# Performance work log

Measured on AMD Instinct MI355X. Metric: run time of the kernel, lower is better.

## Reference

```python
import jax, jax.numpy as jnp
import numpy as np
import math

B, S, E = 2, 4096, 2048
H, HKV, DK, DV = 16, 4, 128, 128
WIN = 512
EPS = 1e-5
NEG = -1e30


def setup_inputs() -> dict:
    key = jax.random.key(0)
    ks = jax.random.split(key, 8)
    scale = 1.0 / math.sqrt(E)
    return {
        "embeddings": jax.random.normal(ks[0], (B, S, E), dtype=jnp.float32),
        "cos_buffer": jax.random.uniform(ks[1], (2, 1, S, DK), dtype=jnp.float32),
        "sin_buffer": jax.random.uniform(ks[2], (2, 1, S, DK), dtype=jnp.float32),
        "wq": jax.random.normal(ks[3], (E, H * DK), dtype=jnp.float32) * scale,
        "wk": jax.random.normal(ks[4], (E, HKV * DK), dtype=jnp.float32) * scale,
        "wv": jax.random.normal(ks[5], (E, HKV * DV), dtype=jnp.float32) * scale,
        "wo": jax.random.normal(ks[6], (H * DV, E), dtype=jnp.float32) * (1.0 / math.sqrt(H * DV)),
        "window_size": WIN,
    }


def _rotate(f, cos, sin):
    half = f.shape[-1] // 2
    swapped = jnp.concatenate([f[..., half:], f[..., :half]], axis=-1)
    return cos * f + sin * swapped


def reference(embeddings, cos_buffer, sin_buffer, wq, wk, wv, wo, window_size):
    b, s, _ = embeddings.shape
    normed = embeddings * jax.lax.rsqrt(
        jnp.mean(jnp.square(embeddings), axis=-1, keepdims=True) + EPS)
    q = (normed @ wq).reshape(b, s, H, DK).transpose(0, 2, 1, 3)
    k = (normed @ wk).reshape(b, s, HKV, DK).transpose(0, 2, 1, 3)
    v = (normed @ wv).reshape(b, s, HKV, DV).transpose(0, 2, 1, 3)

    q = _rotate(q, cos_buffer[0], sin_buffer[0])
    k = _rotate(k, cos_buffer[1], sin_buffer[1])

    g = H // HKV
    k = jnp.repeat(k, g, axis=1)
    v = jnp.repeat(v, g, axis=1)

    W = window_size
    nb = s // W
    qb = q.reshape(b, H, nb, W, DK)
    kb = k.reshape(b, H, nb, W, DK)
    vb = v.reshape(b, H, nb, W, DV)
    k_prev = jnp.pad(kb, ((0, 0), (0, 0), (1, 0), (0, 0), (0, 0)))[:, :, :nb]
    v_prev = jnp.pad(vb, ((0, 0), (0, 0), (1, 0), (0, 0), (0, 0)))[:, :, :nb]
    kcat = jnp.concatenate([k_prev, kb], axis=3)
    vcat = jnp.concatenate([v_prev, vb], axis=3)

    scores = jnp.einsum('bhnqd,bhnkd->bhnqk', qb, kcat) / math.sqrt(DK)

    i = jnp.arange(W)[:, None]
    j = jnp.arange(2 * W)[None, :]
    base = (j > i) & (j <= i + W)
    blk = jnp.arange(nb)[:, None, None]
    mask = base[None] & ((blk > 0) | (j[None] >= W))
    scores = jnp.where(mask[None, None], scores, NEG)

    probs = jax.nn.softmax(scores, axis=-1)
    out = jnp.einsum('bhnqk,bhnkd->bhnqd', probs, vcat)
    out = out.reshape(b, H, s, DV).transpose(0, 2, 1, 3).reshape(b, s, H * DV)
    out = out @ wo
    return embeddings + out
```

## Files before the change

kernel.cpp:

```cpp
#include <hip/hip_runtime.h>

typedef unsigned short u16;
typedef __attribute__((ext_vector_type(8))) short s16x8;
typedef __attribute__((ext_vector_type(8))) unsigned short u16x8;
typedef __attribute__((ext_vector_type(4))) unsigned short u16x4;
typedef __attribute__((ext_vector_type(4))) float f32x4;

#define DEV __device__ __forceinline__

DEV u16 f2bf(float x) {
  union { float f; unsigned u; } c; c.f = x;
  unsigned r = c.u + 0x7FFFu + ((c.u >> 16) & 1u);
  return (u16)(r >> 16);
}
DEV float bf2f(u16 u) {
  union { unsigned u; float f; } c; c.u = ((unsigned)u) << 16;
  return c.f;
}
DEV void gload_lds16(const void* g, void* l) {
  __builtin_amdgcn_global_load_lds((const __attribute__((address_space(1))) void*)g,
                                   (__attribute__((address_space(3))) void*)l, 16, 0, 0);
}

__global__ __launch_bounds__(256) void k_rmsnorm(const float* __restrict__ emb, u16* __restrict__ X) {
  const int row = blockIdx.x;
  const int t = threadIdx.x;
  const float4* p4 = (const float4*)(emb + (size_t)row * 2048);
  float4 v0 = p4[t * 2], v1 = p4[t * 2 + 1];
  float ss = v0.x * v0.x + v0.y * v0.y + v0.z * v0.z + v0.w * v0.w
           + v1.x * v1.x + v1.y * v1.y + v1.z * v1.z + v1.w * v1.w;
  for (int off = 32; off; off >>= 1) ss += __shfl_xor(ss, off);
  __shared__ float red[4];
  if ((t & 63) == 0) red[t >> 6] = ss;
  __syncthreads();
  float tot = red[0] + red[1] + red[2] + red[3];
  float inv = rsqrtf(tot * (1.0f / 2048.0f) + 1e-5f);
  float v[8] = {v0.x, v0.y, v0.z, v0.w, v1.x, v1.y, v1.z, v1.w};
  u16x8 o;
  for (int j = 0; j < 8; ++j) o[j] = f2bf(v[j] * inv);
  *(u16x8*)(X + (size_t)row * 2048 + t * 8) = o;
}

__global__ __launch_bounds__(256) void k_transpose(const float* __restrict__ src, u16* __restrict__ dst,
                                                   int C, int dstStride) {
  __shared__ float tile[32][33];
  const int bc = blockIdx.x * 32, br = blockIdx.y * 32;
  const int tx = threadIdx.x & 31, ty = threadIdx.x >> 5;
  for (int i = 0; i < 32; i += 8)
    tile[ty + i][tx] = src[(size_t)(br + ty + i) * C + bc + tx];
  __syncthreads();
  for (int i = 0; i < 32; i += 8)
    dst[(size_t)(bc + ty + i) * dstStride + br + tx] = f2bf(tile[tx][ty + i]);
}

template <int EPI>
__global__ __launch_bounds__(512) void k_gemm256(const u16* __restrict__ A, const u16* __restrict__ Bt,
                                                 const int N, const int K, const int NBN,
                                                 const float* __restrict__ cosb, const float* __restrict__ sinb,
                                                 u16* __restrict__ Qb, u16* __restrict__ Kb,
                                                 u16* __restrict__ VtOut,
                                                 const float* __restrict__ Emb, float* __restrict__ Cf) {
  __shared__ u16 Asm[2][256 * 64];
  __shared__ u16 Bsm[2][256 * 64];
  const int t = threadIdx.x, w = t >> 6, l = t & 63, g = (l >> 4), cc = l & 15;
  const int wm = w >> 2, wn = w & 3;

  const int lin = blockIdx.x;
  const int bm = lin / NBN, bn = lin % NBN;
  const size_t m0 = (size_t)bm * 256, n0 = (size_t)bn * 256;

  const int srow = t >> 3, sch = t & 7;

  auto stA = [&](int kt, int p, int pass) {
    const int row = pass * 64 + srow;
    const int c2 = sch ^ (row & 7);
    gload_lds16(A + (m0 + row) * K + kt * 64 + c2 * 8, &Asm[p][row * 64 + sch * 8]);
  };
  auto stB = [&](int kt, int p, int pass) {
    const int row = pass * 64 + srow;
    const int c2 = sch ^ (row & 7);
    gload_lds16(Bt + (n0 + row) * K + kt * 64 + c2 * 8, &Bsm[p][row * 64 + sch * 8]);
  };

  f32x4 acc[8][4];
#pragma unroll
  for (int mi = 0; mi < 8; ++mi)
#pragma unroll
    for (int ni = 0; ni < 4; ++ni) acc[mi][ni] = (f32x4){0.f, 0.f, 0.f, 0.f};

  const int NT = K >> 6;
#pragma unroll
  for (int pass = 0; pass < 4; ++pass) { stA(0, 0, pass); stB(0, 0, pass); }
  __syncthreads();

  for (int kt = 0; kt < NT; ++kt) {
    const int p = kt & 1;
    const bool pf = (kt + 1 < NT);
    const u16* Ap = &Asm[p][0];
    const u16* Bp = &Bsm[p][0];

    s16x8 bf[2][4];
#pragma unroll
    for (int kk = 0; kk < 2; ++kk)
#pragma unroll
      for (int ni = 0; ni < 4; ++ni) {
        const int row = wn * 16 + ni * 64 + cc;
        bf[kk][ni] = *(const s16x8*)&Bp[row * 64 + (((kk * 4 + g) ^ (row & 7)) * 8)];
      }

#pragma unroll
    for (int q = 0; q < 4; ++q) {
      s16x8 af[2][2];
#pragma unroll
      for (int kk = 0; kk < 2; ++kk)
#pragma unroll
        for (int m2 = 0; m2 < 2; ++m2) {
          const int row = wm * 128 + (q * 2 + m2) * 16 + cc;
          af[kk][m2] = *(const s16x8*)&Ap[row * 64 + (((kk * 4 + g) ^ (row & 7)) * 8)];
        }
      if (pf) {
        if (q == 0) { stA(kt + 1, p ^ 1, 0); stA(kt + 1, p ^ 1, 1); stB(kt + 1, p ^ 1, 0); }
        else if (q == 1) { stA(kt + 1, p ^ 1, 2); stA(kt + 1, p ^ 1, 3); stB(kt + 1, p ^ 1, 1); }
        else if (q == 2) { stB(kt + 1, p ^ 1, 2); stB(kt + 1, p ^ 1, 3); }
      }
#pragma unroll
      for (int m2 = 0; m2 < 2; ++m2)
#pragma unroll
        for (int ni = 0; ni < 4; ++ni)
#pragma unroll
          for (int kk = 0; kk < 2; ++kk)
            acc[q * 2 + m2][ni] =
                __builtin_amdgcn_mfma_f32_16x16x32_bf16(af[kk][m2], bf[kk][ni], acc[q * 2 + m2][ni], 0, 0, 0);
    }
    __syncthreads();
  }

  if (EPI == 1) {
#pragma unroll
    for (int mi = 0; mi < 8; ++mi)
#pragma unroll
      for (int ni = 0; ni < 4; ++ni)
#pragma unroll
        for (int r = 0; r < 4; ++r) {
          const size_t row = m0 + wm * 128 + mi * 16 + g * 4 + r;
          const size_t col = n0 + wn * 16 + ni * 64 + cc;
          Cf[row * N + col] = acc[mi][ni][r] + Emb[row * N + col];
        }
  } else if ((int)n0 < 2560) {
    const bool isK = (int)n0 >= 2048;
    const float* cbase = cosb + (isK ? 524288 : 0);
    const float* sbase = sinb + (isK ? 524288 : 0);
    const int dlo = wn * 16 + cc;
#pragma unroll
    for (int mi = 0; mi < 8; ++mi)
#pragma unroll
      for (int p = 0; p < 2; ++p) {
        const int colbase = (int)n0 + p * 128;
#pragma unroll
        for (int r = 0; r < 4; ++r) {
          const int row = (int)m0 + wm * 128 + mi * 16 + g * 4 + r;
          const int bb = row >> 12, s = row & 4095;
          const float lo = acc[mi][2 * p + 0][r];
          const float hi = acc[mi][2 * p + 1][r];
          const float* cpr = cbase + (size_t)s * 128;
          const float* spr = sbase + (size_t)s * 128;
          const u16 olo = f2bf(cpr[dlo] * lo + spr[dlo] * hi);
          const u16 ohi = f2bf(cpr[dlo + 64] * hi + spr[dlo + 64] * lo);
          if (!isK) {
            const int h = colbase >> 7;
            u16* dq = Qb + ((size_t)(bb * 16 + h) * 4096 + s) * 128;
            dq[dlo] = olo;
            dq[dlo + 64] = ohi;
          } else {
            const int hkv = (colbase - 2048) >> 7;
            u16* dk = Kb + ((size_t)(bb * 4 + hkv) * 4096 + s) * 128;
            dk[dlo] = olo;
            dk[dlo + 64] = ohi;
          }
        }
      }
  } else {
    const int bb = (int)(m0 >> 12);
    const int s0base = (int)(m0 & 4095);
#pragma unroll
    for (int mi = 0; mi < 8; ++mi)
#pragma unroll
      for (int ni = 0; ni < 4; ++ni) {
        const int dcol = (int)(n0 - 2560) + wn * 16 + ni * 64 + cc;
        const int hkv = dcol >> 7, d = dcol & 127;
        const int s = s0base + wm * 128 + mi * 16 + g * 4;
        u16x4 o;
#pragma unroll
        for (int r = 0; r < 4; ++r) o[r] = f2bf(acc[mi][ni][r]);
        *(u16x4*)(VtOut + ((size_t)(bb * 4 + hkv) * 128 + d) * 4096 + s) = o;
      }
  }
}

__global__ __launch_bounds__(256) void k_attn(const u16* __restrict__ Q, const u16* __restrict__ K,
                                              const u16* __restrict__ Vt, u16* __restrict__ AO) {
  const int bid = blockIdx.x;
  const int lin = (bid & 7) * 128 + (bid >> 3);
  const int grp = lin >> 7;
  const int b = grp >> 2, hkv = grp & 3;
  const int rem = lin & 127;
  const int h = hkv * 4 + (rem >> 5);
  const int qt = rem & 31;

  const int t = threadIdx.x, w = t >> 6, l = t & 63, g = l >> 4, cc = l & 15;
  const int q0 = qt * 128;
  const int myq0 = q0 + w * 32;
  const u16* Qp = Q + (((size_t)b * 16 + h) * 4096 + q0) * 128;
  const u16* Kp = K + ((size_t)b * 4 + hkv) * 4096 * 128;
  const u16* Vp = Vt + ((size_t)b * 4 + hkv) * 128 * 4096;

  __shared__ u16 Kl[2][32 * 128];
  __shared__ u16 Vl[2][128 * 32];
  __shared__ u16 Ps[4][32 * 40];
  u16* myPs = &Ps[w][0];

  auto stage = [&](int kt, int bufi) {
    for (int pass = 0; pass < 2; ++pass) {
      const int m = pass * 256 + t;
      const int row = m >> 4, cst = m & 15;
      const int cor = cst ^ (row & 7);
      gload_lds16(Kp + (size_t)(kt * 32 + row) * 128 + cor * 8, &Kl[bufi][m * 8]);
    }
    for (int pass = 0; pass < 2; ++pass) {
      const int m = pass * 256 + t;
      const int d = m >> 2, cst = m & 3;
      const int cor = cst ^ (d & 3);
      gload_lds16(Vp + (size_t)d * 4096 + kt * 32 + cor * 8, &Vl[bufi][m * 8]);
    }
  };

  s16x8 qf[2][4];
  for (int mi = 0; mi < 2; ++mi)
    for (int kk = 0; kk < 4; ++kk)
      qf[mi][kk] = *(const s16x8*)(Qp + (size_t)(w * 32 + mi * 16 + cc) * 128 + kk * 32 + g * 8);

  f32x4 accO[2][8];
  for (int mi = 0; mi < 2; ++mi)
    for (int nd = 0; nd < 8; ++nd) accO[mi][nd] = (f32x4){0.f, 0.f, 0.f, 0.f};
  float mrun[2], lrun[2];
  for (int mi = 0; mi < 2; ++mi) { mrun[mi] = -1e30f; lrun[mi] = 0.f; }

  int lo = q0 - 511; if (lo < 0) lo = 0;
  const int kt_lo = lo >> 5, kt_hi = (q0 + 127) >> 5;
  const float scale = 0.08838834764831845f;

  int cur = 0;
  stage(kt_lo, 0);
  __syncthreads();

  for (int kt = kt_lo; kt <= kt_hi; ++kt) {
    if (kt < kt_hi) stage(kt + 1, cur ^ 1);

    const int k0 = kt * 32;
    const bool haswork = (k0 <= myq0 + 31) && (k0 + 31 >= myq0 - 511);
    const bool fullw   = (k0 + 31 <= myq0) && (k0 >= myq0 - 480);

    if (haswork) {
      f32x4 sc[2][2];
      for (int mi = 0; mi < 2; ++mi)
        for (int nk = 0; nk < 2; ++nk) sc[mi][nk] = (f32x4){0.f, 0.f, 0.f, 0.f};
      __builtin_amdgcn_s_setprio(1);
      for (int kk = 0; kk < 4; ++kk) {
        s16x8 kb[2];
        for (int nk = 0; nk < 2; ++nk) {
          const int row = nk * 16 + cc;
          kb[nk] = *(const s16x8*)&Kl[cur][row * 128 + (((kk * 4 + g) ^ (row & 7)) * 8)];
        }
        for (int mi = 0; mi < 2; ++mi)
          for (int nk = 0; nk < 2; ++nk)
            sc[mi][nk] = __builtin_amdgcn_mfma_f32_16x16x32_bf16(kb[nk], qf[mi][kk], sc[mi][nk], 0, 0, 0);
      }
      __builtin_amdgcn_s_setprio(0);

      for (int mi = 0; mi < 2; ++mi) {
        const int qpos = myq0 + mi * 16 + cc;
        if (fullw) {
          for (int nk = 0; nk < 2; ++nk)
            for (int r = 0; r < 4; ++r) sc[mi][nk][r] *= scale;
        } else {
          for (int nk = 0; nk < 2; ++nk)
            for (int r = 0; r < 4; ++r) {
              const int kpos = k0 + nk * 16 + g * 4 + r;
              const float v = sc[mi][nk][r] * scale;
              sc[mi][nk][r] = (kpos <= qpos && kpos + 512 > qpos) ? v : -1e30f;
            }
        }
        float rm = sc[mi][0][0];
        for (int nk = 0; nk < 2; ++nk)
          for (int r = 0; r < 4; ++r) rm = fmaxf(rm, sc[mi][nk][r]);
        rm = fmaxf(rm, __shfl_xor(rm, 16));
        rm = fmaxf(rm, __shfl_xor(rm, 32));
        const float mnew = fmaxf(mrun[mi], rm);
        float rs = 0.f;
        if (fullw) {
          for (int nk = 0; nk < 2; ++nk)
            for (int r = 0; r < 4; ++r) {
              float pv = __expf(sc[mi][nk][r] - mnew);
              sc[mi][nk][r] = pv;
              rs += pv;
            }
        } else {
          for (int nk = 0; nk < 2; ++nk)
            for (int r = 0; r < 4; ++r) {
              float pv = sc[mi][nk][r];
              pv = (pv <= -1e29f) ? 0.f : __expf(pv - mnew);
              sc[mi][nk][r] = pv;
              rs += pv;
            }
        }
        rs += __shfl_xor(rs, 16);
        rs += __shfl_xor(rs, 32);
        const float alpha = __expf(mrun[mi] - mnew);
        mrun[mi] = mnew;
        lrun[mi] = lrun[mi] * alpha + rs;
        for (int nd = 0; nd < 8; ++nd)
          for (int r = 0; r < 4; ++r) accO[mi][nd][r] *= alpha;
        for (int nk = 0; nk < 2; ++nk) {
          u16x4 o;
          for (int r = 0; r < 4; ++r) o[r] = f2bf(sc[mi][nk][r]);
          *(u16x4*)&myPs[(mi * 16 + cc) * 40 + nk * 16 + g * 4] = o;
        }
      }

      __builtin_amdgcn_s_setprio(1);
      {
        s16x8 pa[2];
        for (int mi = 0; mi < 2; ++mi)
          pa[mi] = *(const s16x8*)&myPs[(mi * 16 + cc) * 40 + g * 8];
        for (int nd = 0; nd < 8; ++nd) {
          const int d = nd * 16 + cc;
          s16x8 vb = *(const s16x8*)&Vl[cur][d * 32 + ((g ^ (d & 3)) * 8)];
          for (int mi = 0; mi < 2; ++mi)
            accO[mi][nd] = __builtin_amdgcn_mfma_f32_16x16x32_bf16(vb, pa[mi], accO[mi][nd], 0, 0, 0);
        }
      }
      __builtin_amdgcn_s_setprio(0);
    }

    __syncthreads();
    cur ^= 1;
  }

  u16* op = AO + ((size_t)b * 4096 + q0) * 2048 + (size_t)h * 128;
  for (int mi = 0; mi < 2; ++mi) {
    const float inv = 1.0f / lrun[mi];
    for (int nd = 0; nd < 8; ++nd) {
      u16x4 o;
      for (int r = 0; r < 4; ++r) o[r] = f2bf(accO[mi][nd][r] * inv);
      *(u16x4*)(op + (size_t)(w * 32 + mi * 16 + cc) * 2048 + nd * 16 + g * 4) = o;
    }
  }
}

extern "C" void kernel_launch(void* const* d_in, const int* in_sizes, int n_in,
                              void* d_out, int out_size, void* d_ws, size_t ws_size,
                              hipStream_t stream) {
  const float* emb  = (const float*)d_in[0];
  const float* cosb = (const float*)d_in[1];
  const float* sinb = (const float*)d_in[2];
  const float* wq   = (const float*)d_in[3];
  const float* wk   = (const float*)d_in[4];
  const float* wv   = (const float*)d_in[5];
  const float* wo   = (const float*)d_in[6];
  float* out = (float*)d_out;

  char* ws = (char*)d_ws;
  size_t off = 0;
  auto alloc = [&](size_t bytes) -> void* {
    void* p = ws + off;
    off += (bytes + 255) & ~(size_t)255;
    return p;
  };
  u16* X   = (u16*)alloc((size_t)8192 * 2048 * 2);
  u16* Wt  = (u16*)alloc((size_t)3072 * 2048 * 2);
  u16* Wot = (u16*)alloc((size_t)2048 * 2048 * 2);
  u16* Qb  = (u16*)alloc((size_t)2 * 16 * 4096 * 128 * 2);
  u16* Kb  = (u16*)alloc((size_t)2 * 4 * 4096 * 128 * 2);
  u16* VtB = (u16*)alloc((size_t)2 * 4 * 128 * 4096 * 2);
  u16* AOb = X;

  k_transpose<<<dim3(64, 64), 256, 0, stream>>>(wq, Wt, 2048, 2048);
  k_transpose<<<dim3(16, 64), 256, 0, stream>>>(wk, Wt + (size_t)2048 * 2048, 512, 2048);
  k_transpose<<<dim3(16, 64), 256, 0, stream>>>(wv, Wt + (size_t)2560 * 2048, 512, 2048);
  k_transpose<<<dim3(64, 64), 256, 0, stream>>>(wo, Wot, 2048, 2048);
  k_rmsnorm<<<8192, 256, 0, stream>>>(emb, X);
  k_gemm256<0><<<dim3(384), 512, 0, stream>>>(X, Wt, 3072, 2048, 12, cosb, sinb, Qb, Kb, VtB,
                                              nullptr, nullptr);
  k_attn<<<dim3(1024), 256, 0, stream>>>(Qb, Kb, VtB, AOb);
  k_gemm256<1><<<dim3(256), 512, 0, stream>>>(AOb, Wot, 2048, 2048, 8, nullptr, nullptr, nullptr, nullptr,
                                              nullptr, emb, out);
}
```

Before: 338.2 us.

## Replace per-tile syncthreads with fine-grained vmcnt waits and per-quarter barriers in GEMM

The GEMM main loop now stages the next K-tile in four half-tile chunks, one per MFMA quarter, and waits on vmcnt counts instead of a full __syncthreads at the end of each tile. It adds s_setprio around the MFMA groups and explicit sched_barriers so that LDS loads, global-to-LDS copies and MFMAs interleave across waves. The aim is to hide load latency and cut barrier stalls. The cost is more barriers per tile and hand-written waitcnt logic that is fragile: the chosen vmcnt(2) and the buffer reuse timing have to match the number of loads actually in flight.

Result: slower. 359.3 us (+6.3%).

```diff
diff --git a/kernel.cpp b/kernel.cpp
--- a/kernel.cpp
+++ b/kernel.cpp
@@ -71,16 +71,18 @@
 
   const int srow = t >> 3, sch = t & 7;
 
-  auto stA = [&](int kt, int p, int pass) {
-    const int row = pass * 64 + srow;
-    const int c2 = sch ^ (row & 7);
-    gload_lds16(A + (m0 + row) * K + kt * 64 + c2 * 8, &Asm[p][row * 64 + sch * 8]);
+  auto stageHalf = [&](int kt, int p, int which) {
+    const u16* src = (which < 2) ? A : Bt;
+    const size_t base0 = (which < 2) ? m0 : n0;
+    u16* lds = (which < 2) ? &Asm[p][0] : &Bsm[p][0];
+    const int h = (which & 1) * 128;
+#pragma unroll
+    for (int pass = 0; pass < 2; ++pass) {
+      const int row = h + pass * 64 + srow;
+      const int c2 = sch ^ (row & 7);
+      gload_lds16(src + (base0 + row) * K + kt * 64 + c2 * 8, lds + row * 64 + sch * 8);
+    }
   };
-  auto stB = [&](int kt, int p, int pass) {
-    const int row = pass * 64 + srow;
-    const int c2 = sch ^ (row & 7);
-    gload_lds16(Bt + (n0 + row) * K + kt * 64 + c2 * 8, &Bsm[p][row * 64 + sch * 8]);
-  };
 
   f32x4 acc[8][4];
 #pragma unroll
@@ -90,8 +92,7 @@
 
   const int NT = K >> 6;
 #pragma unroll
-  for (int pass = 0; pass < 4; ++pass) { stA(0, 0, pass); stB(0, 0, pass); }
-  __syncthreads();
+  for (int h = 0; h < 4; ++h) stageHalf(0, 0, h);
 
   for (int kt = 0; kt < NT; ++kt) {
     const int p = kt & 1;
@@ -101,28 +102,44 @@
 
     s16x8 bf[2][4];
 #pragma unroll
-    for (int kk = 0; kk < 2; ++kk)
-#pragma unroll
-      for (int ni = 0; ni < 4; ++ni) {
-        const int row = wn * 16 + ni * 64 + cc;
-        bf[kk][ni] = *(const s16x8*)&Bp[row * 64 + (((kk * 4 + g) ^ (row & 7)) * 8)];
-      }
-
-#pragma unroll
     for (int q = 0; q < 4; ++q) {
       s16x8 af[2][2];
-#pragma unroll
-      for (int kk = 0; kk < 2; ++kk)
-#pragma unroll
-        for (int m2 = 0; m2 < 2; ++m2) {
-          const int row = wm * 128 + (q * 2 + m2) * 16 + cc;
-          af[kk][m2] = *(const s16x8*)&Ap[row * 64 + (((kk * 4 + g) ^ (row & 7)) * 8)];
-        }
-      if (pf) {
-        if (q == 0) { stA(kt + 1, p ^ 1, 0); stA(kt + 1, p ^ 1, 1); stB(kt + 1, p ^ 1, 0); }
-        else if (q == 1) { stA(kt + 1, p ^ 1, 2); stA(kt + 1, p ^ 1, 3); stB(kt + 1, p ^ 1, 1); }
-        else if (q == 2) { stB(kt + 1, p ^ 1, 2); stB(kt + 1, p ^ 1, 3); }
-      }
+      if (q == 0) {
+        if (pf) {
+          stageHalf(kt + 1, p ^ 1, 0);
+          asm volatile("s_waitcnt vmcnt(2)" ::: "memory");
+        } else {
+          asm volatile("s_waitcnt vmcnt(0)" ::: "memory");
+        }
+        __builtin_amdgcn_s_barrier();
+#pragma unroll
+        for (int kk = 0; kk < 2; ++kk)
+#pragma unroll
+          for (int ni = 0; ni < 4; ++ni) {
+            const int row = wn * 16 + ni * 64 + cc;
+            bf[kk][ni] = *(const s16x8*)&Bp[row * 64 + (((kk * 4 + g) ^ (row & 7)) * 8)];
+          }
+#pragma unroll
+        for (int kk = 0; kk < 2; ++kk)
+#pragma unroll
+          for (int m2 = 0; m2 < 2; ++m2) {
+            const int row = wm * 128 + m2 * 16 + cc;
+            af[kk][m2] = *(const s16x8*)&Ap[row * 64 + (((kk * 4 + g) ^ (row & 7)) * 8)];
+          }
+      } else {
+#pragma unroll
+        for (int kk = 0; kk < 2; ++kk)
+#pragma unroll
+          for (int m2 = 0; m2 < 2; ++m2) {
+            const int row = wm * 128 + (q * 2 + m2) * 16 + cc;
+            af[kk][m2] = *(const s16x8*)&Ap[row * 64 + (((kk * 4 + g) ^ (row & 7)) * 8)];
+          }
+        if (pf) stageHalf(kt + 1, p ^ 1, q);
+        __builtin_amdgcn_s_barrier();
+      }
+      asm volatile("s_waitcnt lgkmcnt(0)" ::: "memory");
+      __builtin_amdgcn_sched_barrier(0);
+      __builtin_amdgcn_s_setprio(1);
 #pragma unroll
       for (int m2 = 0; m2 < 2; ++m2)
 #pragma unroll
@@ -131,8 +148,9 @@
           for (int kk = 0; kk < 2; ++kk)
             acc[q * 2 + m2][ni] =
                 __builtin_amdgcn_mfma_f32_16x16x32_bf16(af[kk][m2], bf[kk][ni], acc[q * 2 + m2][ni], 0, 0, 0);
-    }
-    __syncthreads();
+      __builtin_amdgcn_s_setprio(0);
+      __builtin_amdgcn_s_barrier();
+    }
   }
 
   if (EPI == 1) {
```
